# Kernel tuning notes

Measured on AMD Instinct MI355X. Metric: run time of the kernel, lower is better.

## Reference

```python
import jax, jax.numpy as jnp
import numpy as np

D_MODEL = 1024
NHEAD = 16
D_HEAD = D_MODEL // NHEAD


def setup_inputs() -> dict:
    key = jax.random.key(0)
    ks = jax.random.split(key, 5)
    s_in = 1.0 / np.sqrt(D_MODEL)
    x = jax.random.normal(ks[0], (2, 2048, D_MODEL), dtype=jnp.float32)
    Wqkv = jax.random.uniform(ks[1], (D_MODEL, 3 * D_MODEL), jnp.float32, -s_in, s_in)
    bqkv = jax.random.uniform(ks[2], (3 * D_MODEL,), jnp.float32, -s_in, s_in)
    Wproj = jax.random.uniform(ks[3], (D_MODEL, D_MODEL), jnp.float32, -s_in, s_in)
    bproj = jax.random.uniform(ks[4], (D_MODEL,), jnp.float32, -s_in, s_in)
    return {"x": x, "Wqkv": Wqkv, "bqkv": bqkv, "Wproj": Wproj, "bproj": bproj}


def reference(x, Wqkv, bqkv, Wproj, bproj):
    B, N, D = x.shape
    qkv = x @ Wqkv + bqkv                       # [B, N, 3D]
    q, k, v = jnp.split(qkv, 3, axis=-1)
    # [B, N, D] -> [B, H, N, d]
    def to_heads(t):
        return t.reshape(B, N, NHEAD, D_HEAD).transpose(0, 2, 1, 3)
    q, k, v = to_heads(q), to_heads(k), to_heads(v)
    scale = 1.0 / np.sqrt(D_HEAD).astype(np.float32)
    attn = jnp.einsum('bhqd,bhkd->bhqk', q, k) * scale
    attn = jax.nn.softmax(attn, axis=-1)
    y = jnp.einsum('bhqk,bhkd->bhqd', attn, v)  # [B, H, N, d]
    y = y.transpose(0, 2, 1, 3).reshape(B, N, D)
    return y @ Wproj + bproj
```

## Files before the change

### kernel.cpp

```cpp
#include <hip/hip_runtime.h>
#include <hip/hip_bf16.h>
#include <stdint.h>

typedef __hip_bfloat16 bf16;
typedef __attribute__((ext_vector_type(8))) short short8;
typedef __attribute__((ext_vector_type(4))) float f32x4;

#define QSCALE 0.18033688011f

__device__ __forceinline__ float fast_exp2(float x) {
#if __has_builtin(__builtin_amdgcn_exp2f)
  return __builtin_amdgcn_exp2f(x);
#else
  return exp2f(x);
#endif
}

__device__ __forceinline__ uint32_t pack2_bf16(float a, float b) {
#if __has_builtin(__builtin_amdgcn_cvt_pk_bf16_f32)
  typedef __attribute__((ext_vector_type(2))) __bf16 bf16x2;
  bf16x2 v = __builtin_amdgcn_cvt_pk_bf16_f32(a, b);
  return __builtin_bit_cast(uint32_t, v);
#else
  uint32_t ua = __builtin_bit_cast(uint32_t, a);
  uint32_t ub = __builtin_bit_cast(uint32_t, b);
  ua += 0x7FFF + ((ua >> 16) & 1);
  ub += 0x7FFF + ((ub >> 16) & 1);
  return (ua >> 16) | (ub & 0xFFFF0000u);
#endif
}

__device__ __forceinline__ void gload_lds16(const bf16* g, bf16* l) {
#if __has_builtin(__builtin_amdgcn_global_load_lds)
  __builtin_amdgcn_global_load_lds(
      (const __attribute__((address_space(1))) void*)(uintptr_t)g,
      (__attribute__((address_space(3))) void*)(uint32_t)(uintptr_t)l,
      16, 0, 0);
#else
  int lane = threadIdx.x & 63;
  *(short8*)(l + lane * 8) = *(const short8*)(g + lane * 8);
#endif
}

__device__ __forceinline__ void lds_barrier() {
  asm volatile("s_waitcnt lgkmcnt(0)\n\ts_barrier" ::: "memory");
}

__device__ __forceinline__ void transpose_tile(const float* __restrict__ in,
                                               bf16* __restrict__ out,
                                               int R, int C, int bx, int by,
                                               bf16 (*t)[72]) {
  const int r0 = by * 64, c0 = bx * 64;
  const int rr = threadIdx.x >> 3, cc = (threadIdx.x & 7) * 8;
#pragma unroll
  for (int rep = 0; rep < 2; ++rep) {
    int y = rr + rep * 32;
    const float* p = in + (size_t)(r0 + y) * C + c0 + cc;
    f32x4 v0 = *(const f32x4*)p;
    f32x4 v1 = *(const f32x4*)(p + 4);
#pragma unroll
    for (int j = 0; j < 4; ++j) {
      t[cc + j][y] = __float2bfloat16(v0[j]);
      t[cc + 4 + j][y] = __float2bfloat16(v1[j]);
    }
  }
  __syncthreads();
#pragma unroll
  for (int rep = 0; rep < 2; ++rep) {
    int y = rr + rep * 32;
    short8 v = *(const short8*)&t[y][cc];
    *(short8*)(out + (size_t)(c0 + y) * R + r0 + cc) = v;
  }
}

__global__ __launch_bounds__(256)
void prep_k(const float* __restrict__ x, bf16* __restrict__ xb,
            const float* __restrict__ Wqkv, bf16* __restrict__ WtQkv,
            const float* __restrict__ Wproj, bf16* __restrict__ WtP) {
  __shared__ __align__(16) bf16 t[64][72];
  const int bid = blockIdx.x;
  if (bid < 2048) {
    int i = (bid * 256 + threadIdx.x) * 8;
    f32x4 v0 = *(const f32x4*)(x + i);
    f32x4 v1 = *(const f32x4*)(x + i + 4);
    short8 r;
    bf16* rb = (bf16*)&r;
#pragma unroll
    for (int j = 0; j < 4; ++j) {
      rb[j] = __float2bfloat16(v0[j]);
      rb[4 + j] = __float2bfloat16(v1[j]);
    }
    *(short8*)(xb + i) = r;
  } else if (bid < 2048 + 768) {
    int b = bid - 2048;
    transpose_tile(Wqkv, WtQkv, 1024, 3072, b % 48, b / 48, t);
  } else {
    int b = bid - 2816;
    transpose_tile(Wproj, WtP, 1024, 1024, b % 16, b / 16, t);
  }
}

template <int MODE, int TM>
__global__ __launch_bounds__(256, 2)
void gemm_bt(const bf16* __restrict__ A, const bf16* __restrict__ Bt,
             const float* __restrict__ bias, float* __restrict__ outp,
             bf16* __restrict__ Qd, bf16* __restrict__ Kd, bf16* __restrict__ Vt,
             int M, int Nn, int K) {
  constexpr int MI = TM / 32;
  __shared__ __align__(16) bf16 smem[(TM == 128) ? 9216 : 6144];
  bf16* As = smem;
  bf16* Bs = smem + TM * 32;

  const int tid = threadIdx.x;
  const int wave = tid >> 6, lane = tid & 63;
  const int quad = lane >> 4, l16 = lane & 15;
  const int mw = (wave >> 1) * (TM / 2), nw = (wave & 1) * 64;

  const int nwg = gridDim.x * gridDim.y;
  const int ord = blockIdx.y * gridDim.x + blockIdx.x;
  const int wg = (ord & 7) * (nwg >> 3) + (ord >> 3);
  const int m_blk = (wg / gridDim.x) * TM, n_blk = (wg % gridDim.x) * 128;

  f32x4 acc[MI][4];
#pragma unroll
  for (int i = 0; i < MI; ++i)
#pragma unroll
    for (int j = 0; j < 4; ++j) acc[i][j] = (f32x4){0.f, 0.f, 0.f, 0.f};

  const int rowA = lane >> 2, colA = (lane & 3) * 8;
  const int chunkB = wave * 2;
  const bf16* gB = Bt + (size_t)(n_blk + chunkB * 16 + rowA) * K + colA;
  bf16* lB0 = &Bs[chunkB * 16 * 32];
  bf16* lB1 = &Bs[(chunkB + 1) * 16 * 32];

  const int chunkA = (TM == 128) ? wave * 2 : wave;
  const bf16* gA = A + (size_t)(m_blk + chunkA * 16 + rowA) * K + colA;
  bf16* lA0 = &As[chunkA * 16 * 32];
  bf16* lA1 = &As[(chunkA + 1) * 16 * 32];

  for (int kt = 0; kt < K; kt += 32) {
    gload_lds16(gA, lA0);
    if (TM == 128) gload_lds16(gA + 16 * K, lA1);
    gload_lds16(gB, lB0);
    gload_lds16(gB + 16 * K, lB1);
    gA += 32; gB += 32;
    __syncthreads();
    short8 af[MI], bfv[4];
#pragma unroll
    for (int i = 0; i < MI; ++i)
      af[i] = *(const short8*)&As[(mw + i * 16 + l16) * 32 + quad * 8];
#pragma unroll
    for (int j = 0; j < 4; ++j)
      bfv[j] = *(const short8*)&Bs[(nw + j * 16 + l16) * 32 + quad * 8];
#pragma unroll
    for (int i = 0; i < MI; ++i)
#pragma unroll
      for (int j = 0; j < 4; ++j)
        acc[i][j] = __builtin_amdgcn_mfma_f32_16x16x32_bf16(af[i], bfv[j],
                                                            acc[i][j], 0, 0, 0);
    __syncthreads();
  }

  if (MODE == 0) {
    float bval[4];
#pragma unroll
    for (int j = 0; j < 4; ++j) bval[j] = bias[n_blk + nw + j * 16 + l16];

    const int part = n_blk >> 10;
    const int b = m_blk >> 11;
    const int tloc = m_blk & 2047;
    const int h0 = (n_blk & 1023) >> 6;

#pragma unroll
    for (int p = 0; p < 2; ++p) {
      __syncthreads();
      if ((nw >> 6) == p) {
        if (part == 2) {
#pragma unroll
          for (int i = 0; i < MI; ++i)
#pragma unroll
            for (int j = 0; j < 4; ++j) {
              const int dh = j * 16 + l16;
              const int t0 = mw + i * 16 + quad * 4;
              uint2 pk;
              pk.x = pack2_bf16(acc[i][j][0] + bval[j], acc[i][j][1] + bval[j]);
              pk.y = pack2_bf16(acc[i][j][2] + bval[j], acc[i][j][3] + bval[j]);
              *(uint2*)&smem[dh * 136 + t0] = pk;
            }
        } else {
          const float sc = (part == 0) ? QSCALE : 1.0f;
#pragma unroll
          for (int i = 0; i < MI; ++i)
#pragma unroll
            for (int j = 0; j < 4; ++j) {
              const int d = j * 16 + l16;
              const int t0 = mw + i * 16 + quad * 4;
#pragma unroll
              for (int r = 0; r < 4; ++r)
                smem[(t0 + r) * 72 + d] =
                    __float2bfloat16((acc[i][j][r] + bval[j]) * sc);
            }
        }
      }
      __syncthreads();
      const size_t bh = (size_t)(b * 16 + h0 + p);
      if (part == 2) {
#pragma unroll
        for (int it = 0; it < 4; ++it) {
          const int dl = (tid >> 4) + it * 16;
          const int t8 = (tid & 15) * 8;
          short8 v = *(const short8*)&smem[dl * 136 + t8];
          *(short8*)&Vt[(bh * 64 + dl) * 2048 + tloc + t8] = v;
        }
      } else {
        bf16* dst = (part == 0) ? Qd : Kd;
#pragma unroll
        for (int it = 0; it < 4; ++it) {
          const int row = (tid >> 3) + it * 32;
          const int col8 = (tid & 7) * 8;
          short8 v = *(const short8*)&smem[row * 72 + col8];
          *(short8*)&dst[(bh * 2048 + tloc + row) * 64 + col8] = v;
        }
      }
    }
  } else {
#pragma unroll
    for (int j = 0; j < 4; ++j) {
      const int ncol = n_blk + nw + j * 16 + l16;
      const float bval = bias[ncol];
#pragma unroll
      for (int i = 0; i < MI; ++i) {
        const int mrow0 = m_blk + mw + i * 16 + quad * 4;
#pragma unroll
        for (int r = 0; r < 4; ++r)
          outp[(size_t)(mrow0 + r) * Nn + ncol] = acc[i][j][r] + bval;
      }
    }
  }
}

__global__ __launch_bounds__(256, 4)
void attn_kernel(const bf16* __restrict__ Qg, const bf16* __restrict__ Kg,
                 const bf16* __restrict__ Vt, bf16* __restrict__ yg) {
  __shared__ __align__(16) char pool[36864];
  bf16* KsB = (bf16*)pool;
  bf16* VtsB = (bf16*)(pool + 18432);

  const int tid = threadIdx.x;
  const int wave = tid >> 6, lane = tid & 63;
  const int quad = lane >> 4, l16 = lane & 15;
  const int qh = wave & 1, kvh = wave >> 1;

  const int bx0 = blockIdx.x;
  const int bx = ((bx0 & 7) << 7) | (bx0 >> 3);
  const int qt = bx & 31;
  const int bh = bx >> 5;

  const bf16* Qb = Qg + ((size_t)bh * 2048 + qt * 64) * 64;
  const bf16* Kb = Kg + (size_t)bh * 2048 * 64;
  const bf16* Vtb = Vt + (size_t)bh * 64 * 2048;

  short8 qf[2][2];
#pragma unroll
  for (int qblk = 0; qblk < 2; ++qblk)
#pragma unroll
    for (int ks = 0; ks < 2; ++ks)
      qf[qblk][ks] = *(const short8*)(
          Qb + (size_t)(qh * 32 + qblk * 16 + l16) * 64 + ks * 32 + quad * 8);

  const int kr = tid >> 3, kc = (tid & 7) * 8;
  const int vdd = tid & 63, vo = tid >> 6;
  const int voff0 = vdd * 72 + (((vo) + (vdd >> 3)) & 7) * 8;
  const int voff1 = vdd * 72 + (((vo + 4) + (vdd >> 3)) & 7) * 8;
  const bf16* Kp0 = Kb + (size_t)kr * 64 + kc;
  const bf16* Kp1 = Kb + (size_t)(kr + 32) * 64 + kc;
  const bf16* Vp0 = Vtb + (size_t)vdd * 2048 + vo * 8;
  const bf16* Vp1 = Vtb + (size_t)vdd * 2048 + (vo + 4) * 8;

  {
    short8 a = *(const short8*)Kp0;
    short8 b = *(const short8*)Kp1;
    short8 c = *(const short8*)Vp0;
    short8 d = *(const short8*)Vp1;
    *(short8*)(KsB + kr * 72 + kc) = a;
    *(short8*)(KsB + (kr + 32) * 72 + kc) = b;
    *(short8*)(VtsB + voff0) = c;
    *(short8*)(VtsB + voff1) = d;
  }
  short8 gk0 = *(const short8*)(Kp0 + (size_t)64 * 64);
  short8 gk1 = *(const short8*)(Kp1 + (size_t)64 * 64);
  short8 gv0 = *(const short8*)(Vp0 + 64);
  short8 gv1 = *(const short8*)(Vp1 + 64);
  __syncthreads();

  f32x4 yacc[2][4];
#pragma unroll
  for (int qblk = 0; qblk < 2; ++qblk)
#pragma unroll
    for (int dblk = 0; dblk < 4; ++dblk)
      yacc[qblk][dblk] = (f32x4){0.f, 0.f, 0.f, 0.f};
  f32x4 sum_acc[2];
  sum_acc[0] = (f32x4){0.f, 0.f, 0.f, 0.f};
  sum_acc[1] = (f32x4){0.f, 0.f, 0.f, 0.f};

  uint4 ones_u;
  ones_u.x = ones_u.y = ones_u.z = ones_u.w = 0x3F803F80u;
  const short8 ones8 = __builtin_bit_cast(short8, ones_u);

  const int kfo = (kvh * 32 + l16) * 72 + quad * 8;
  int vbo[4][2];
#pragma unroll
  for (int dblk = 0; dblk < 4; ++dblk) {
    const int d = dblk * 16 + l16;
#pragma unroll
    for (int kvblk = 0; kvblk < 2; ++kvblk) {
      const int c = kvh * 4 + kvblk * 2 + (quad >> 1);
      vbo[dblk][kvblk] = d * 72 + ((c + (d >> 3)) & 7) * 8 + (quad & 1) * 4;
    }
  }

  for (int kt = 0; kt < 2048; kt += 64) {
    const int cur = (kt >> 6) & 1;
    bf16* KsC = KsB + cur * 4608;
    bf16* VtsC = VtsB + cur * 4608;

    if (kt + 64 < 2048) {
      bf16* KsN = KsB + (cur ^ 1) * 4608;
      bf16* VtsN = VtsB + (cur ^ 1) * 4608;
      *(short8*)(KsN + kr * 72 + kc) = gk0;
      *(short8*)(KsN + (kr + 32) * 72 + kc) = gk1;
      *(short8*)(VtsN + voff0) = gv0;
      *(short8*)(VtsN + voff1) = gv1;
      if (kt + 128 < 2048) {
        gk0 = *(const short8*)(Kp0 + (size_t)(kt + 128) * 64);
        gk1 = *(const short8*)(Kp1 + (size_t)(kt + 128) * 64);
        gv0 = *(const short8*)(Vp0 + kt + 128);
        gv1 = *(const short8*)(Vp1 + kt + 128);
      }
    }

    short8 kf[2][2];
#pragma unroll
    for (int kvblk = 0; kvblk < 2; ++kvblk)
#pragma unroll
      for (int ks = 0; ks < 2; ++ks)
        kf[kvblk][ks] =
            *(const short8*)(KsC + kfo + kvblk * 16 * 72 + ks * 32);

    short8 pa8[2];
#pragma unroll
    for (int qblk = 0; qblk < 2; ++qblk) {
      f32x4 s0 = (f32x4){0.f, 0.f, 0.f, 0.f};
      f32x4 s1 = (f32x4){0.f, 0.f, 0.f, 0.f};
      s0 = __builtin_amdgcn_mfma_f32_16x16x32_bf16(kf[0][0], qf[qblk][0], s0, 0, 0, 0);
      s0 = __builtin_amdgcn_mfma_f32_16x16x32_bf16(kf[0][1], qf[qblk][1], s0, 0, 0, 0);
      s1 = __builtin_amdgcn_mfma_f32_16x16x32_bf16(kf[1][0], qf[qblk][0], s1, 0, 0, 0);
      s1 = __builtin_amdgcn_mfma_f32_16x16x32_bf16(kf[1][1], qf[qblk][1], s1, 0, 0, 0);
      float p0 = fast_exp2(s0[0]), p1 = fast_exp2(s0[1]);
      float p2 = fast_exp2(s0[2]), p3 = fast_exp2(s0[3]);
      float p4 = fast_exp2(s1[0]), p5 = fast_exp2(s1[1]);
      float p6 = fast_exp2(s1[2]), p7 = fast_exp2(s1[3]);
      uint4 u;
      u.x = pack2_bf16(p0, p1);
      u.y = pack2_bf16(p2, p3);
      u.z = pack2_bf16(p4, p5);
      u.w = pack2_bf16(p6, p7);
      pa8[qblk] = __builtin_bit_cast(short8, u);
      sum_acc[qblk] = __builtin_amdgcn_mfma_f32_16x16x32_bf16(
          pa8[qblk], ones8, sum_acc[qblk], 0, 0, 0);
    }

#pragma unroll
    for (int dblk = 0; dblk < 4; ++dblk) {
      uint2 lo = *(const uint2*)(VtsC + vbo[dblk][0]);
      uint2 hi = *(const uint2*)(VtsC + vbo[dblk][1]);
      uint4 u;
      u.x = lo.x; u.y = lo.y; u.z = hi.x; u.w = hi.y;
      short8 vb8 = __builtin_bit_cast(short8, u);
      yacc[0][dblk] = __builtin_amdgcn_mfma_f32_16x16x32_bf16(
          pa8[0], vb8, yacc[0][dblk], 0, 0, 0);
      yacc[1][dblk] = __builtin_amdgcn_mfma_f32_16x16x32_bf16(
          pa8[1], vb8, yacc[1][dblk], 0, 0, 0);
    }

    lds_barrier();
  }

  __syncthreads();
  float* red = (float*)pool;
  float* sred = (float*)(pool + 16384);
  if (kvh == 1) {
#pragma unroll
    for (int qblk = 0; qblk < 2; ++qblk) {
#pragma unroll
      for (int dblk = 0; dblk < 4; ++dblk) {
        const int f = (qh * 2 + qblk) * 4 + dblk;
        *(f32x4*)&red[(f * 64 + quad * 16 + l16) * 4] = yacc[qblk][dblk];
      }
      if (l16 == 0)
        *(f32x4*)&sred[(qh * 2 + qblk) * 16 + quad * 4] = sum_acc[qblk];
    }
  }
  __syncthreads();
  if (kvh == 0) {
    const int b = bh >> 4, h = bh & 15;
    const size_t rowbase = (size_t)b * 2048 + qt * 64;
#pragma unroll
    for (int qblk = 0; qblk < 2; ++qblk) {
      f32x4 sp = *(const f32x4*)&sred[(qh * 2 + qblk) * 16 + quad * 4];
#pragma unroll
      for (int dblk = 0; dblk < 4; ++dblk) {
        const int f = (qh * 2 + qblk) * 4 + dblk;
        f32x4 o = *(const f32x4*)&red[(f * 64 + quad * 16 + l16) * 4];
#pragma unroll
        for (int r = 0; r < 4; ++r) yacc[qblk][dblk][r] += o[r];
      }
#pragma unroll
      for (int r = 0; r < 4; ++r) {
        const float inv = 1.f / (sum_acc[qblk][r] + sp[r]);
        const int rr = qh * 32 + qblk * 16 + quad * 4 + r;
#pragma unroll
        for (int dblk = 0; dblk < 4; ++dblk)
          yg[(rowbase + rr) * 1024 + h * 64 + dblk * 16 + l16] =
              __float2bfloat16(yacc[qblk][dblk][r] * inv);
      }
    }
  }
}

extern "C" void kernel_launch(void* const* d_in, const int* in_sizes, int n_in,
                              void* d_out, int out_size, void* d_ws, size_t ws_size,
                              hipStream_t stream) {
  const float* x = (const float*)d_in[0];
  const float* Wqkv = (const float*)d_in[1];
  const float* bqkv = (const float*)d_in[2];
  const float* Wproj = (const float*)d_in[3];
  const float* bproj = (const float*)d_in[4];
  float* out = (float*)d_out;

  if (ws_size < (size_t)40 * 1024 * 1024) return;

  char* ws = (char*)d_ws;
  bf16* xb    = (bf16*)(ws + 0);
  bf16* yd    = (bf16*)(ws + 0);
  bf16* WtQkv = (bf16*)(ws + 8388608);
  bf16* WtP   = (bf16*)(ws + 14680064);
  bf16* Qd    = (bf16*)(ws + 16777216);
  bf16* Kd    = (bf16*)(ws + 25165824);
  bf16* Vten  = (bf16*)(ws + 33554432);

  prep_k<<<3072, 256, 0, stream>>>(x, xb, Wqkv, WtQkv, Wproj, WtP);
  gemm_bt<0, 128><<<dim3(24, 32), 256, 0, stream>>>(
      xb, WtQkv, bqkv, nullptr, Qd, Kd, Vten, 4096, 3072, 1024);
  attn_kernel<<<dim3(1024), 256, 0, stream>>>(Qd, Kd, Vten, yd);
  gemm_bt<1, 64><<<dim3(8, 64), 256, 0, stream>>>(
      yd, WtP, bproj, out, nullptr, nullptr, nullptr, 4096, 1024, 1024);
}
```

Before: 192.4 us.

## Pre-swizzle K/Vt in QKV epilogue and load attention tiles via global_load_lds

The QKV GEMM epilogue now writes K and Vt with an XOR swizzle baked into global memory. The attention kernel can then copy 64x64 tiles straight into LDS with direct global-to-LDS loads instead of staging them through registers, and reads them back with XOR-swizzled offsets. This drops the register staging, lets the unpadded LDS buffers shrink, and raises the occupancy hint for the TM=128 GEMM. In exchange, each iteration now waits on vmcnt(0) before the barrier, so prefetch latency is exposed within a single iteration instead of being hidden across two.

```diff
diff --git a/kernel.cpp b/kernel.cpp
--- a/kernel.cpp
+++ b/kernel.cpp
@@ -42,10 +42,6 @@
 #endif
 }
 
-__device__ __forceinline__ void lds_barrier() {
-  asm volatile("s_waitcnt lgkmcnt(0)\n\ts_barrier" ::: "memory");
-}
-
 __device__ __forceinline__ void transpose_tile(const float* __restrict__ in,
                                                bf16* __restrict__ out,
                                                int R, int C, int bx, int by,
@@ -101,7 +97,7 @@
 }
 
 template <int MODE, int TM>
-__global__ __launch_bounds__(256, 2)
+__global__ __launch_bounds__(256, (TM == 128) ? 3 : 2)
 void gemm_bt(const bf16* __restrict__ A, const bf16* __restrict__ Bt,
              const float* __restrict__ bias, float* __restrict__ outp,
              bf16* __restrict__ Qd, bf16* __restrict__ Kd, bf16* __restrict__ Vt,
@@ -209,8 +205,9 @@
         for (int it = 0; it < 4; ++it) {
           const int dl = (tid >> 4) + it * 16;
           const int t8 = (tid & 15) * 8;
+          const int t8s = (t8 & 64) | ((t8 ^ ((dl & 7) << 3)) & 63);
           short8 v = *(const short8*)&smem[dl * 136 + t8];
-          *(short8*)&Vt[(bh * 64 + dl) * 2048 + tloc + t8] = v;
+          *(short8*)&Vt[(bh * 64 + dl) * 2048 + tloc + t8s] = v;
         }
       } else {
         bf16* dst = (part == 0) ? Qd : Kd;
@@ -218,8 +215,9 @@
         for (int it = 0; it < 4; ++it) {
           const int row = (tid >> 3) + it * 32;
           const int col8 = (tid & 7) * 8;
+          const int c8 = (part == 1) ? (col8 ^ ((row & 7) << 3)) : col8;
           short8 v = *(const short8*)&smem[row * 72 + col8];
-          *(short8*)&dst[(bh * 2048 + tloc + row) * 64 + col8] = v;
+          *(short8*)&dst[(bh * 2048 + tloc + row) * 64 + c8] = v;
         }
       }
     }
@@ -242,9 +240,9 @@
 __global__ __launch_bounds__(256, 4)
 void attn_kernel(const bf16* __restrict__ Qg, const bf16* __restrict__ Kg,
                  const bf16* __restrict__ Vt, bf16* __restrict__ yg) {
-  __shared__ __align__(16) char pool[36864];
+  __shared__ __align__(16) char pool[32768];
   bf16* KsB = (bf16*)pool;
-  bf16* VtsB = (bf16*)(pool + 18432);
+  bf16* VtsB = (bf16*)(pool + 16384);
 
   const int tid = threadIdx.x;
   const int wave = tid >> 6, lane = tid & 63;
@@ -268,30 +266,35 @@
       qf[qblk][ks] = *(const short8*)(
           Qb + (size_t)(qh * 32 + qblk * 16 + l16) * 64 + ks * 32 + quad * 8);
 
-  const int kr = tid >> 3, kc = (tid & 7) * 8;
-  const int vdd = tid & 63, vo = tid >> 6;
-  const int voff0 = vdd * 72 + (((vo) + (vdd >> 3)) & 7) * 8;
-  const int voff1 = vdd * 72 + (((vo + 4) + (vdd >> 3)) & 7) * 8;
-  const bf16* Kp0 = Kb + (size_t)kr * 64 + kc;
-  const bf16* Kp1 = Kb + (size_t)(kr + 32) * 64 + kc;
-  const bf16* Vp0 = Vtb + (size_t)vdd * 2048 + vo * 8;
-  const bf16* Vp1 = Vtb + (size_t)vdd * 2048 + (vo + 4) * 8;
-
-  {
-    short8 a = *(const short8*)Kp0;
-    short8 b = *(const short8*)Kp1;
-    short8 c = *(const short8*)Vp0;
-    short8 d = *(const short8*)Vp1;
-    *(short8*)(KsB + kr * 72 + kc) = a;
-    *(short8*)(KsB + (kr + 32) * 72 + kc) = b;
-    *(short8*)(VtsB + voff0) = c;
-    *(short8*)(VtsB + voff1) = d;
-  }
-  short8 gk0 = *(const short8*)(Kp0 + (size_t)64 * 64);
-  short8 gk1 = *(const short8*)(Kp1 + (size_t)64 * 64);
-  short8 gv0 = *(const short8*)(Vp0 + 64);
-  short8 gv1 = *(const short8*)(Vp1 + 64);
-  __syncthreads();
+  const int sj = wave * 2;
+  const bf16* kg = Kb + sj * 512 + lane * 8;
+  const bf16* vg = Vtb + (size_t)(sj * 8 + (lane >> 3)) * 2048 +
+                   (lane & 7) * 8;
+
+  int kfo[2][2];
+#pragma unroll
+  for (int kvblk = 0; kvblk < 2; ++kvblk)
+#pragma unroll
+    for (int ks = 0; ks < 2; ++ks)
+      kfo[kvblk][ks] = (kvh * 32 + kvblk * 16 + l16) * 64 +
+                       (((ks * 4 + quad) ^ (l16 & 7)) << 3);
+  int vbo[4][2];
+#pragma unroll
+  for (int dblk = 0; dblk < 4; ++dblk) {
+    const int d = dblk * 16 + l16;
+#pragma unroll
+    for (int kvblk = 0; kvblk < 2; ++kvblk) {
+      const int ct = kvh * 4 + kvblk * 2 + (quad >> 1);
+      vbo[dblk][kvblk] = d * 64 + ((ct ^ (d & 7)) << 3) + (quad & 1) * 4;
+    }
+  }
+
+#pragma unroll
+  for (int j = 0; j < 2; ++j) {
+    gload_lds16(kg + j * 512, KsB + sj * 512 + j * 512);
+    gload_lds16(vg + (size_t)j * 16384, VtsB + sj * 512 + j * 512);
+  }
+  asm volatile("s_waitcnt vmcnt(0) lgkmcnt(0)\n\ts_barrier" ::: "memory");
 
   f32x4 yacc[2][4];
 #pragma unroll
@@ -307,45 +310,27 @@
   ones_u.x = ones_u.y = ones_u.z = ones_u.w = 0x3F803F80u;
   const short8 ones8 = __builtin_bit_cast(short8, ones_u);
 
-  const int kfo = (kvh * 32 + l16) * 72 + quad * 8;
-  int vbo[4][2];
-#pragma unroll
-  for (int dblk = 0; dblk < 4; ++dblk) {
-    const int d = dblk * 16 + l16;
-#pragma unroll
-    for (int kvblk = 0; kvblk < 2; ++kvblk) {
-      const int c = kvh * 4 + kvblk * 2 + (quad >> 1);
-      vbo[dblk][kvblk] = d * 72 + ((c + (d >> 3)) & 7) * 8 + (quad & 1) * 4;
-    }
-  }
-
   for (int kt = 0; kt < 2048; kt += 64) {
     const int cur = (kt >> 6) & 1;
-    bf16* KsC = KsB + cur * 4608;
-    bf16* VtsC = VtsB + cur * 4608;
 
     if (kt + 64 < 2048) {
-      bf16* KsN = KsB + (cur ^ 1) * 4608;
-      bf16* VtsN = VtsB + (cur ^ 1) * 4608;
-      *(short8*)(KsN + kr * 72 + kc) = gk0;
-      *(short8*)(KsN + (kr + 32) * 72 + kc) = gk1;
-      *(short8*)(VtsN + voff0) = gv0;
-      *(short8*)(VtsN + voff1) = gv1;
-      if (kt + 128 < 2048) {
-        gk0 = *(const short8*)(Kp0 + (size_t)(kt + 128) * 64);
-        gk1 = *(const short8*)(Kp1 + (size_t)(kt + 128) * 64);
-        gv0 = *(const short8*)(Vp0 + kt + 128);
-        gv1 = *(const short8*)(Vp1 + kt + 128);
-      }
-    }
+      bf16* Kd = KsB + (cur ^ 1) * 4096;
+      bf16* Vd = VtsB + (cur ^ 1) * 4096;
+#pragma unroll
+      for (int j = 0; j < 2; ++j) {
+        gload_lds16(kg + (kt + 64) * 64 + j * 512, Kd + sj * 512 + j * 512);
+        gload_lds16(vg + kt + 64 + (size_t)j * 16384, Vd + sj * 512 + j * 512);
+      }
+    }
+    const bf16* KsC = KsB + cur * 4096;
+    const bf16* VtsC = VtsB + cur * 4096;
 
     short8 kf[2][2];
 #pragma unroll
     for (int kvblk = 0; kvblk < 2; ++kvblk)
 #pragma unroll
       for (int ks = 0; ks < 2; ++ks)
-        kf[kvblk][ks] =
-            *(const short8*)(KsC + kfo + kvblk * 16 * 72 + ks * 32);
+        kf[kvblk][ks] = *(const short8*)(KsC + kfo[kvblk][ks]);
 
     short8 pa8[2];
 #pragma unroll
@@ -383,7 +368,7 @@
           pa8[1], vb8, yacc[1][dblk], 0, 0, 0);
     }
 
-    lds_barrier();
+    asm volatile("s_waitcnt vmcnt(0) lgkmcnt(0)\n\ts_barrier" ::: "memory");
   }
 
   __syncthreads();
```

New measurement: 186.5 us. 3.1% less time.
